# Kernel tuning notes

Hardware: AMD Instinct MI355X
Metric: run time of the kernel (lower is better)

## Reference

```python
import jax, jax.numpy as jnp
import numpy as np

TEMP = 1.0
EULER_GAMMA = 0.5772156649015329
BIG = 1.0e9


def setup_inputs() -> dict:
    key = jax.random.key(0)
    k = jax.random.split(key, 8)
    B, N, D, H = 32, 1024, 1024, 512  # batch, seq, d_model, hidden_size//2
    queries = jax.random.normal(k[0], (B, N, D), jnp.float32)
    queries_mask = jnp.ones((B, N), dtype=bool)
    W1 = jax.random.normal(k[1], (D, H), jnp.float32) * 0.02
    b1 = jnp.zeros((H,), jnp.float32)
    W2 = jax.random.normal(k[2], (H, 1), jnp.float32) * 0.02
    b2 = jnp.zeros((1,), jnp.float32)
    uniform_noise = jax.random.uniform(k[3], (B, N, 1), jnp.float32, 0.0, 1e-5)
    gumbel_noise = jax.random.gumbel(k[4], (B, N, 1), jnp.float32)
    return {"queries": queries, "queries_mask": queries_mask, "W1": W1, "b1": b1,
            "W2": W2, "b2": b2, "uniform_noise": uniform_noise,
            "gumbel_noise": gumbel_noise, "action_refinement": 1}


def reference(queries, queries_mask, W1, b1, W2, b2, uniform_noise, gumbel_noise, action_refinement):
    B, N, D = queries.shape
    # block0: Dense(H, relu) -> Dense(1); then softplus clamp + log + tiny uniform noise
    h = jax.nn.relu(jnp.einsum('bnd,dh->bnh', queries, W1) + b1)
    acts = jnp.einsum('bnh,ho->bno', h, W2) + b2                      # [B,N,1]
    acts = jnp.log(jnp.maximum(jax.nn.softplus(acts), 1e-5)) + uniform_noise
    acts = jnp.repeat(acts, action_refinement, axis=0)                # [BR,N,1]
    vmask = jnp.repeat(queries_mask[:, None, :].astype(jnp.float32), action_refinement, axis=0)  # [BR,1,N]
    n_valid = jnp.sum(vmask, axis=-1)                                 # [BR,1]
    mask_n1 = jnp.transpose(vmask, (0, 2, 1))                         # [BR,N,1]
    sqz_mask = mask_n1[..., 0]                                        # [BR,N]
    masked_acts = jnp.where(mask_n1 > 0, acts, -1e6)                  # [BR,N,1]
    perturb = masked_acts + gumbel_noise                              # [BR,N,1]
    # deterministic NeuralSort
    s = (jnp.exp(perturb) * mask_n1)[..., 0]                          # [BR,N]
    A = jnp.abs(s[:, :, None] - s[:, None, :])                        # [BR,N,N]
    Bmat = jnp.sum(A, axis=-1, keepdims=True)                         # A @ (1 1^T): row sums broadcast
    scaling = (N + 1 - 2 * (jnp.arange(N) + 1)).astype(jnp.float32)   # [N]
    C = s[:, :, None] * scaling[None, None, :]                        # [BR,N,N]
    P_hat = jnp.transpose(C - Bmat, (0, 2, 1)) - (1.0 - vmask) * BIG  # [BR,N,N]
    # greedy argmax permutation extraction (find_permu), vectorized over batch
    BR = P_hat.shape[0]
    def step(flag, row):                                              # row: [BR,N]
        tmp = row - flag * BIG
        idx = jnp.argmax(tmp, axis=-1)
        flag = jnp.maximum(flag, jax.nn.one_hot(idx, N, dtype=flag.dtype))
        return flag, idx
    _, idxs = jax.lax.scan(step, jnp.zeros((BR, N), jnp.float32), jnp.transpose(P_hat, (1, 0, 2)))
    chosen = jnp.transpose(idxs).astype(jnp.int32)                    # [BR,N]
    chosen = jnp.concatenate([jnp.zeros((BR, 1), jnp.int32), chosen[:, :-1]], axis=-1)
    id_permu = jnp.arange(N, dtype=jnp.int32)[None, :]
    permu = jnp.where(sqz_mask > 0, chosen, id_permu)                 # [BR,N]
    sample_permu = jax.nn.one_hot(permu, N, axis=-1, dtype=jnp.float32)
    # Plackett-Luce log-likelihood of sampled permutation
    exp_actis = jnp.exp(jnp.take_along_axis(masked_acts[..., 0], permu, axis=-1))
    rev_cumsum = jnp.cumsum(exp_actis[:, ::-1], axis=-1)[:, ::-1]
    eps = 1e-20
    log_nom = (jnp.log(exp_actis + eps) - jnp.log(rev_cumsum + eps)) * sqz_mask
    log_nom = jnp.sum(log_nom, axis=-1, keepdims=True)                # [BR,1]
    log_norm = jnp.zeros_like(log_nom)
    # KL term
    sqz_acts = acts[..., 0]
    kl1 = n_valid * (np.log(TEMP) - 1.0 + EULER_GAMMA * (1.0 / TEMP - 1.0))
    s1 = (1.0 / TEMP) * jnp.sum(sqz_acts * sqz_mask, axis=-1).reshape(-1, 1)
    s2 = jnp.sum(jnp.exp(-1.0 / TEMP * jnp.maximum(sqz_acts * sqz_mask, -20.0 * TEMP)), axis=-1).reshape(-1, 1) - (jnp.float32(N) - n_valid)
    kl = kl1 + s1 + s2 * jnp.exp(jax.lax.lgamma(jnp.float32(1.0 + 1.0 / TEMP)))
    return sample_permu, masked_acts[..., 0], kl, log_nom, log_norm
```

## Files before the change

### kernel.cpp

```cpp
#include <hip/hip_runtime.h>
#include <math.h>

#define BB 32
#define NN 1024
#define DD 1024
#define HH 512

#define OUT0_OFF 0
#define OUT1_OFF (BB * NN * NN)
#define OUT2_OFF (OUT1_OFF + BB * NN)
#define OUT3_OFF (OUT2_OFF + BB)
#define OUT4_OFF (OUT3_OFF + BB)

#define WS_ACTS 0
#define WS_W1T  131072
#define WS_RANK 1179648

typedef __attribute__((ext_vector_type(8))) short short8;
typedef __attribute__((ext_vector_type(4))) float floatx4;

__device__ inline unsigned int f2bf(float x) {
    unsigned int u = __builtin_bit_cast(unsigned int, x);
    return (u + 0x7FFFu + ((u >> 16) & 1u)) >> 16;
}

__global__ __launch_bounds__(1024) void w1t_kernel(const float* __restrict__ W1,
                                                   unsigned short* __restrict__ W1T)
{
    __shared__ float T[32][33];
    const int tx = threadIdx.x, ty = threadIdx.y;
    const int d0 = blockIdx.x * 32, h0 = blockIdx.y * 32;
    T[ty][tx] = W1[(d0 + ty) * HH + h0 + tx];
    __syncthreads();
    W1T[(size_t)(h0 + ty) * DD + d0 + tx] = (unsigned short)f2bf(T[tx][ty]);
}

#define ASTRIDE 40
__global__ __launch_bounds__(256, 2) void gemm_acts_kernel(
    const float* __restrict__ q, const unsigned short* __restrict__ W1T,
    const float* __restrict__ b1, const float* __restrict__ W2,
    const float* __restrict__ b2, const float* __restrict__ unoise,
    float* __restrict__ acts_ws, float* __restrict__ out1)
{
    __shared__ short As[64 * ASTRIDE];
    __shared__ short Bs[512 * ASTRIDE];
    __shared__ float red[64][4];

    const int tid = threadIdx.x;
    const int w = tid >> 6;
    const int lane = tid & 63;
    const int c = lane & 15;
    const int qd = lane >> 4;
    const int m0 = blockIdx.x * 64;

    float b1v[8], w2v[8];
    #pragma unroll
    for (int tn = 0; tn < 8; ++tn) {
        int col = w * 128 + tn * 16 + c;
        b1v[tn] = b1[col];
        w2v[tn] = W2[col];
    }

    floatx4 acc[8][4];
    #pragma unroll
    for (int tn = 0; tn < 8; ++tn)
        #pragma unroll
        for (int tm = 0; tm < 4; ++tm)
            acc[tn][tm] = (floatx4){0.f, 0.f, 0.f, 0.f};

    const int am = tid >> 2;
    const int akf = (tid & 3) * 8;
    const float* aptr = q + (size_t)(m0 + am) * DD + akf;

    const uint4* w1t4 = (const uint4*)W1T;

    for (int kk = 0; kk < 32; ++kk) {
        __syncthreads();
        {
            const float4* ap = (const float4*)(aptr + kk * 32);
            float4 v0 = ap[0], v1 = ap[1];
            uint4 pk;
            pk.x = f2bf(v0.x) | (f2bf(v0.y) << 16);
            pk.y = f2bf(v0.z) | (f2bf(v0.w) << 16);
            pk.z = f2bf(v1.x) | (f2bf(v1.y) << 16);
            pk.w = f2bf(v1.z) | (f2bf(v1.w) << 16);
            *(uint4*)(&As[am * ASTRIDE + akf]) = pk;
        }
        #pragma unroll
        for (int i = 0; i < 8; ++i) {
            int f = i * 256 + tid;
            int n = f >> 2, kp = f & 3;
            uint4 v = w1t4[(size_t)n * 128 + kk * 4 + kp];
            *(uint4*)(&Bs[n * ASTRIDE + kp * 8]) = v;
        }
        __syncthreads();
        short8 af[4];
        #pragma unroll
        for (int tm = 0; tm < 4; ++tm)
            af[tm] = *(const short8*)(&As[(tm * 16 + c) * ASTRIDE + qd * 8]);
        #pragma unroll
        for (int tn = 0; tn < 8; ++tn) {
            short8 bf = *(const short8*)(&Bs[(w * 128 + tn * 16 + c) * ASTRIDE + qd * 8]);
            #pragma unroll
            for (int tm = 0; tm < 4; ++tm)
                acc[tn][tm] = __builtin_amdgcn_mfma_f32_16x16x32_bf16(
                    af[tm], bf, acc[tn][tm], 0, 0, 0);
        }
    }

    #pragma unroll
    for (int tm = 0; tm < 4; ++tm) {
        #pragma unroll
        for (int r = 0; r < 4; ++r) {
            float p = 0.f;
            #pragma unroll
            for (int tn = 0; tn < 8; ++tn) {
                float v = acc[tn][tm][r] + b1v[tn];
                p = fmaf(fmaxf(v, 0.f), w2v[tn], p);
            }
            p += __shfl_xor(p, 1);
            p += __shfl_xor(p, 2);
            p += __shfl_xor(p, 4);
            p += __shfl_xor(p, 8);
            if (c == 0) red[tm * 16 + qd * 4 + r][w] = p;
        }
    }
    __syncthreads();
    if (tid < 64) {
        float raw = red[tid][0] + red[tid][1] + red[tid][2] + red[tid][3] + b2[0];
        float sp = fmaxf(raw, 0.f) + log1pf(expf(-fabsf(raw)));
        int row = m0 + tid;
        float av = logf(fmaxf(sp, 1e-5f)) + unoise[row];
        acts_ws[row] = av;
        out1[row]    = av;
    }
}

__global__ __launch_bounds__(256) void zero_kernel(float4* __restrict__ p, int n4)
{
    int idx = blockIdx.x * blockDim.x + threadIdx.x;
    int stride = gridDim.x * blockDim.x;
    float4 z = make_float4(0.f, 0.f, 0.f, 0.f);
    for (int i = idx; i < n4; i += stride) p[i] = z;
}

__global__ __launch_bounds__(256) void rank_kernel(
    const float* __restrict__ acts_ws, const float* __restrict__ gumbel,
    int* __restrict__ rank)
{
    __shared__ float P[NN];
    const int b = blockIdx.x >> 2;
    const int chunk = blockIdx.x & 3;
    const int tid = threadIdx.x;
    #pragma unroll
    for (int r = 0; r < 4; ++r) {
        int j = r * 256 + tid;
        P[j] = acts_ws[b * NN + j] + gumbel[b * NN + j];
    }
    __syncthreads();
    const int i = chunk * 256 + tid;
    const float pert = P[i];
    int cnt = 0;
    const float4* P4 = (const float4*)P;
    for (int j4 = 0; j4 < NN / 4; ++j4) {
        float4 pv = P4[j4];
        int j = j4 * 4;
        cnt += (pv.x > pert) || (pv.x == pert && j + 0 < i);
        cnt += (pv.y > pert) || (pv.y == pert && j + 1 < i);
        cnt += (pv.z > pert) || (pv.z == pert && j + 2 < i);
        cnt += (pv.w > pert) || (pv.w == pert && j + 3 < i);
    }
    rank[b * NN + i] = cnt;
}

__global__ __launch_bounds__(1024) void permu_stats_kernel(
    const float* __restrict__ acts_ws, const int* __restrict__ rank,
    float* __restrict__ out0, float* __restrict__ out2,
    float* __restrict__ out3, float* __restrict__ out4)
{
    __shared__ float A[NN];
    __shared__ int   IDX[NN];
    __shared__ float S[NN];
    __shared__ float R[NN];

    const int b = blockIdx.x;
    const int i = threadIdx.x;

    float a = acts_ws[b * NN + i];
    A[i] = a;
    IDX[rank[b * NN + i]] = i;
    __syncthreads();

    int perm = (i == 0) ? 0 : IDX[i - 1];
    out0[((size_t)b * NN + i) * NN + perm] = 1.0f;

    float e = expf(A[perm]);
    S[i] = e;
    __syncthreads();
    #pragma unroll
    for (int off = 1; off < NN; off <<= 1) {
        float v = (i + off < NN) ? S[i + off] : 0.f;
        __syncthreads();
        S[i] += v;
        __syncthreads();
    }
    float term = logf(e + 1e-20f) - logf(S[i] + 1e-20f);

    float lognom = 0.f, s1 = 0.f;
    R[i] = term;
    __syncthreads();
    #pragma unroll
    for (int off = 512; off > 0; off >>= 1) {
        if (i < off) R[i] += R[i + off];
        __syncthreads();
    }
    if (i == 0) lognom = R[0];
    R[i] = a;
    __syncthreads();
    #pragma unroll
    for (int off = 512; off > 0; off >>= 1) {
        if (i < off) R[i] += R[i + off];
        __syncthreads();
    }
    if (i == 0) s1 = R[0];
    R[i] = expf(-fmaxf(a, -20.f));
    __syncthreads();
    #pragma unroll
    for (int off = 512; off > 0; off >>= 1) {
        if (i < off) R[i] += R[i + off];
        __syncthreads();
    }
    if (i == 0) {
        float s2 = R[0];
        out2[b] = -(float)NN + s1 + s2;
        out3[b] = lognom;
        out4[b] = 0.f;
    }
}

extern "C" void kernel_launch(void* const* d_in, const int* in_sizes, int n_in,
                              void* d_out, int out_size, void* d_ws, size_t ws_size,
                              hipStream_t stream)
{
    const float* q      = (const float*)d_in[0];
    const float* W1     = (const float*)d_in[2];
    const float* b1     = (const float*)d_in[3];
    const float* W2     = (const float*)d_in[4];
    const float* b2     = (const float*)d_in[5];
    const float* unoise = (const float*)d_in[6];
    const float* gumbel = (const float*)d_in[7];

    float* out  = (float*)d_out;
    char*  ws   = (char*)d_ws;
    float*          acts = (float*)(ws + WS_ACTS);
    unsigned short* W1T  = (unsigned short*)(ws + WS_W1T);
    int*            rank = (int*)(ws + WS_RANK);

    w1t_kernel<<<dim3(32, 16), dim3(32, 32), 0, stream>>>(W1, W1T);
    gemm_acts_kernel<<<(BB * NN) / 64, 256, 0, stream>>>(q, W1T, b1, W2, b2,
                                                         unoise, acts,
                                                         out + OUT1_OFF);
    zero_kernel<<<8192, 256, 0, stream>>>((float4*)(out + OUT0_OFF),
                                          (BB * NN * NN) / 4);
    rank_kernel<<<BB * 4, 256, 0, stream>>>(acts, gumbel, rank);
    permu_stats_kernel<<<BB, 1024, 0, stream>>>(acts, rank,
                                                out + OUT0_OFF, out + OUT2_OFF,
                                                out + OUT3_OFF, out + OUT4_OFF);
}
```

Before: 325.5 us.

## Enlarge GEMM row tile, prefetch next K-slice into registers, use wave-shuffle scans

The fused MLP GEMM now processes 128 rows per block with 512 threads arranged as a 2x4 warp grid. Each W1 tile loaded into shared memory is therefore reused across twice as many rows, and the next K-slice of queries and weights is prefetched into registers while the MFMAs run on the current one. The permutation/statistics kernel replaces its shared-memory Hillis-Steele suffix scan and three tree reductions with wave-level shuffles plus a small cross-wave step, removing many block barriers. The costs are higher register pressure and half as many GEMM blocks (256), which may lower occupancy on a many-CU GPU.

Result: slower. 377.8 us (+16.1%).

```diff
diff --git a/kernel.cpp b/kernel.cpp
--- a/kernel.cpp
+++ b/kernel.cpp
@@ -36,30 +36,25 @@
 }
 
 #define ASTRIDE 40
-__global__ __launch_bounds__(256, 2) void gemm_acts_kernel(
+#define MT 128
+__global__ __launch_bounds__(512, 2) void gemm_acts_kernel(
     const float* __restrict__ q, const unsigned short* __restrict__ W1T,
     const float* __restrict__ b1, const float* __restrict__ W2,
     const float* __restrict__ b2, const float* __restrict__ unoise,
     float* __restrict__ acts_ws, float* __restrict__ out1)
 {
-    __shared__ short As[64 * ASTRIDE];
-    __shared__ short Bs[512 * ASTRIDE];
-    __shared__ float red[64][4];
+    __shared__ short As[MT * ASTRIDE];
+    __shared__ short Bs[HH * ASTRIDE];
+    __shared__ float red[MT][4];
 
     const int tid = threadIdx.x;
     const int w = tid >> 6;
     const int lane = tid & 63;
     const int c = lane & 15;
     const int qd = lane >> 4;
-    const int m0 = blockIdx.x * 64;
-
-    float b1v[8], w2v[8];
-    #pragma unroll
-    for (int tn = 0; tn < 8; ++tn) {
-        int col = w * 128 + tn * 16 + c;
-        b1v[tn] = b1[col];
-        w2v[tn] = W2[col];
-    }
+    const int wr = (w >> 2) * 64;
+    const int wc = (w & 3) * 128;
+    const int m0 = blockIdx.x * MT;
 
     floatx4 acc[8][4];
     #pragma unroll
@@ -68,46 +63,65 @@
         for (int tm = 0; tm < 4; ++tm)
             acc[tn][tm] = (floatx4){0.f, 0.f, 0.f, 0.f};
 
-    const int am = tid >> 2;
-    const int akf = (tid & 3) * 8;
-    const float* aptr = q + (size_t)(m0 + am) * DD + akf;
-
+    const int srow = tid >> 2;
+    const int skp  = tid & 3;
+    const float* aptr = q + (size_t)(m0 + srow) * DD + skp * 8;
     const uint4* w1t4 = (const uint4*)W1T;
 
+    float4 a0, a1;
+    uint4 bv[4];
+
+    {
+        const float4* ap = (const float4*)aptr;
+        a0 = ap[0]; a1 = ap[1];
+        #pragma unroll
+        for (int ii = 0; ii < 4; ++ii)
+            bv[ii] = w1t4[(size_t)(ii * 128 + srow) * 128 + skp];
+    }
+
+    #pragma unroll 1
     for (int kk = 0; kk < 32; ++kk) {
+        {
+            uint4 pk;
+            pk.x = f2bf(a0.x) | (f2bf(a0.y) << 16);
+            pk.y = f2bf(a0.z) | (f2bf(a0.w) << 16);
+            pk.z = f2bf(a1.x) | (f2bf(a1.y) << 16);
+            pk.w = f2bf(a1.z) | (f2bf(a1.w) << 16);
+            *(uint4*)(&As[srow * ASTRIDE + skp * 8]) = pk;
+            #pragma unroll
+            for (int ii = 0; ii < 4; ++ii)
+                *(uint4*)(&Bs[(ii * 128 + srow) * ASTRIDE + skp * 8]) = bv[ii];
+        }
         __syncthreads();
-        {
-            const float4* ap = (const float4*)(aptr + kk * 32);
-            float4 v0 = ap[0], v1 = ap[1];
-            uint4 pk;
-            pk.x = f2bf(v0.x) | (f2bf(v0.y) << 16);
-            pk.y = f2bf(v0.z) | (f2bf(v0.w) << 16);
-            pk.z = f2bf(v1.x) | (f2bf(v1.y) << 16);
-            pk.w = f2bf(v1.z) | (f2bf(v1.w) << 16);
-            *(uint4*)(&As[am * ASTRIDE + akf]) = pk;
-        }
-        #pragma unroll
-        for (int i = 0; i < 8; ++i) {
-            int f = i * 256 + tid;
-            int n = f >> 2, kp = f & 3;
-            uint4 v = w1t4[(size_t)n * 128 + kk * 4 + kp];
-            *(uint4*)(&Bs[n * ASTRIDE + kp * 8]) = v;
-        }
-        __syncthreads();
+        if (kk < 31) {
+            const float4* ap = (const float4*)(aptr + (kk + 1) * 32);
+            a0 = ap[0]; a1 = ap[1];
+            #pragma unroll
+            for (int ii = 0; ii < 4; ++ii)
+                bv[ii] = w1t4[(size_t)(ii * 128 + srow) * 128 + (kk + 1) * 4 + skp];
+        }
         short8 af[4];
         #pragma unroll
         for (int tm = 0; tm < 4; ++tm)
-            af[tm] = *(const short8*)(&As[(tm * 16 + c) * ASTRIDE + qd * 8]);
+            af[tm] = *(const short8*)(&As[(wr + tm * 16 + c) * ASTRIDE + qd * 8]);
         #pragma unroll
         for (int tn = 0; tn < 8; ++tn) {
-            short8 bf = *(const short8*)(&Bs[(w * 128 + tn * 16 + c) * ASTRIDE + qd * 8]);
+            short8 bf = *(const short8*)(&Bs[(wc + tn * 16 + c) * ASTRIDE + qd * 8]);
             #pragma unroll
             for (int tm = 0; tm < 4; ++tm)
                 acc[tn][tm] = __builtin_amdgcn_mfma_f32_16x16x32_bf16(
                     af[tm], bf, acc[tn][tm], 0, 0, 0);
         }
-    }
-
+        __syncthreads();
+    }
+
+    float b1v[8], w2v[8];
+    #pragma unroll
+    for (int tn = 0; tn < 8; ++tn) {
+        int col = wc + tn * 16 + c;
+        b1v[tn] = b1[col];
+        w2v[tn] = W2[col];
+    }
     #pragma unroll
     for (int tm = 0; tm < 4; ++tm) {
         #pragma unroll
@@ -122,11 +136,11 @@
             p += __shfl_xor(p, 2);
             p += __shfl_xor(p, 4);
             p += __shfl_xor(p, 8);
-            if (c == 0) red[tm * 16 + qd * 4 + r][w] = p;
-        }
-    }
-    __syncthreads();
-    if (tid < 64) {
+            if (c == 0) red[wr + tm * 16 + qd * 4 + r][w & 3] = p;
+        }
+    }
+    __syncthreads();
+    if (tid < MT) {
         float raw = red[tid][0] + red[tid][1] + red[tid][2] + red[tid][3] + b2[0];
         float sp = fmaxf(raw, 0.f) + log1pf(expf(-fabsf(raw)));
         int row = m0 + tid;
@@ -180,11 +194,14 @@
 {
     __shared__ float A[NN];
     __shared__ int   IDX[NN];
-    __shared__ float S[NN];
-    __shared__ float R[NN];
+    __shared__ float WT[16];
+    __shared__ float WSUF[17];
+    __shared__ float P0[16], P1[16], P2[16];
 
     const int b = blockIdx.x;
     const int i = threadIdx.x;
+    const int lane = i & 63;
+    const int w = i >> 6;
 
     float a = acts_ws[b * NN + i];
     A[i] = a;
@@ -195,45 +212,44 @@
     out0[((size_t)b * NN + i) * NN + perm] = 1.0f;
 
     float e = expf(A[perm]);
-    S[i] = e;
-    __syncthreads();
-    #pragma unroll
-    for (int off = 1; off < NN; off <<= 1) {
-        float v = (i + off < NN) ? S[i + off] : 0.f;
-        __syncthreads();
-        S[i] += v;
-        __syncthreads();
-    }
-    float term = logf(e + 1e-20f) - logf(S[i] + 1e-20f);
-
-    float lognom = 0.f, s1 = 0.f;
-    R[i] = term;
-    __syncthreads();
-    #pragma unroll
-    for (int off = 512; off > 0; off >>= 1) {
-        if (i < off) R[i] += R[i + off];
-        __syncthreads();
-    }
-    if (i == 0) lognom = R[0];
-    R[i] = a;
-    __syncthreads();
-    #pragma unroll
-    for (int off = 512; off > 0; off >>= 1) {
-        if (i < off) R[i] += R[i + off];
-        __syncthreads();
-    }
-    if (i == 0) s1 = R[0];
-    R[i] = expf(-fmaxf(a, -20.f));
-    __syncthreads();
-    #pragma unroll
-    for (int off = 512; off > 0; off >>= 1) {
-        if (i < off) R[i] += R[i + off];
-        __syncthreads();
-    }
+    float s = e;
+    #pragma unroll
+    for (int off = 1; off < 64; off <<= 1) {
+        float v = __shfl_down(s, off);
+        if (lane + off < 64) s += v;
+    }
+    if (lane == 0) WT[w] = s;
+    __syncthreads();
+    if (w == 0) {
+        float t = (lane < 16) ? WT[lane] : 0.f;
+        #pragma unroll
+        for (int off = 1; off < 16; off <<= 1) {
+            float v = __shfl_down(t, off);
+            if (lane + off < 16) t += v;
+        }
+        if (lane < 16) WSUF[lane] = t;
+        if (lane == 0) WSUF[16] = 0.f;
+    }
+    __syncthreads();
+
+    float S = s + WSUF[w + 1];
+    float term = logf(e + 1e-20f) - logf(S + 1e-20f);
+
+    float r0 = term, r1 = a, r2 = expf(-fmaxf(a, -20.f));
+    #pragma unroll
+    for (int off = 1; off < 64; off <<= 1) {
+        r0 += __shfl_xor(r0, off);
+        r1 += __shfl_xor(r1, off);
+        r2 += __shfl_xor(r2, off);
+    }
+    if (lane == 0) { P0[w] = r0; P1[w] = r1; P2[w] = r2; }
+    __syncthreads();
     if (i == 0) {
-        float s2 = R[0];
-        out2[b] = -(float)NN + s1 + s2;
-        out3[b] = lognom;
+        float t0 = 0.f, t1 = 0.f, t2 = 0.f;
+        #pragma unroll
+        for (int k = 0; k < 16; ++k) { t0 += P0[k]; t1 += P1[k]; t2 += P2[k]; }
+        out3[b] = t0;
+        out2[b] = -(float)NN + t1 + t2;
         out4[b] = 0.f;
     }
 }
@@ -257,7 +273,7 @@
     int*            rank = (int*)(ws + WS_RANK);
 
     w1t_kernel<<<dim3(32, 16), dim3(32, 32), 0, stream>>>(W1, W1T);
-    gemm_acts_kernel<<<(BB * NN) / 64, 256, 0, stream>>>(q, W1T, b1, W2, b2,
+    gemm_acts_kernel<<<(BB * NN) / MT, 512, 0, stream>>>(q, W1T, b1, W2, b2,
                                                          unoise, acts,
                                                          out + OUT1_OFF);
     zero_kernel<<<8192, 256, 0, stream>>>((float4*)(out + OUT0_OFF),
```
